# Optimization experiments

Measured on AMD Instinct MI355X. Metric: run time of the kernel, lower is better.

The kernel has to match this reference:

```python
import jax, jax.numpy as jnp
import numpy as np

B, S, D, H = 1, 4096, 1024, 16
HD = D // H  # head_dim = 64


def setup_inputs() -> dict:
    key = jax.random.key(0)
    k1, k2, k3 = jax.random.split(key, 3)
    scale = 0.02
    return {
        "x": jax.random.normal(k1, (B, S, D), dtype=jnp.float32),
        "w_qkv": jax.random.normal(k2, (D, 3 * D), dtype=jnp.float32) * scale,
        "b_qkv": jnp.zeros((3 * D,), dtype=jnp.float32),
        "w_proj": jax.random.normal(k3, (D, D), dtype=jnp.float32) * scale,
        "b_proj": jnp.zeros((D,), dtype=jnp.float32),
    }


def reference(x, w_qkv, b_qkv, w_proj, b_proj):
    b, s, d = x.shape
    qkv = x @ w_qkv + b_qkv                      # [b, s, 3d]
    q, k, v = jnp.split(qkv, 3, axis=-1)
    # [b, h, s, hd]
    q = q.reshape(b, s, H, HD).transpose(0, 2, 1, 3)
    k = k.reshape(b, s, H, HD).transpose(0, 2, 1, 3)
    v = v.reshape(b, s, H, HD).transpose(0, 2, 1, 3)
    score = jnp.einsum("bhqd,bhkd->bhqk", q, k) / jnp.sqrt(jnp.float32(HD))
    causal = jnp.tril(jnp.ones((s, s), dtype=bool))
    score = jnp.where(causal, score, -jnp.inf)
    attn = jax.nn.softmax(score, axis=-1)        # dropout omitted (eval mode, p effectively 0)
    out = jnp.einsum("bhqk,bhkd->bhqd", attn, v)  # [b, h, s, hd]
    out = out.transpose(0, 2, 1, 3).reshape(b, s, d)
    return out @ w_proj + b_proj
```

## Files before the change

kernel.cpp:

```cpp
#include <hip/hip_runtime.h>
#include <hip/hip_bf16.h>
#include <math.h>

typedef __bf16 bf16;
typedef __bf16 bf16x8 __attribute__((ext_vector_type(8)));
typedef __bf16 bf16x4 __attribute__((ext_vector_type(4)));
typedef float f32x4 __attribute__((ext_vector_type(4)));

#define S_ 4096
#define D_ 1024
#define H_ 16
#define HD_ 64
#define N3_ 3072
#define NSPLIT 4

typedef const __attribute__((address_space(1))) void* gas1_t;
typedef __attribute__((address_space(3))) void* las3_t;
static __device__ __forceinline__ void g2l16(const void* g, void* l) {
  __builtin_amdgcn_global_load_lds((gas1_t)g, (las3_t)l, 16, 0, 0);
}

__global__ __launch_bounds__(256) void prep_kernel(const float* __restrict__ x,
                                                   bf16* __restrict__ xb,
                                                   const float* __restrict__ w_qkv,
                                                   bf16* __restrict__ wqkvT,
                                                   const float* __restrict__ w_proj,
                                                   bf16* __restrict__ wprojT) {
  __shared__ float t[32][33];
  const int b = blockIdx.x;
  if (b < 4096) {
    int i = (b * 256 + threadIdx.x) * 4;
    float4 v = *(const float4*)(x + i);
    bf16x4 o;
    o.x = (bf16)v.x; o.y = (bf16)v.y; o.z = (bf16)v.z; o.w = (bf16)v.w;
    *(bf16x4*)(xb + i) = o;
    return;
  }
  const float* in; bf16* outp; int ldin, bx, by;
  if (b < 7168) { int b2 = b - 4096; in = w_qkv;  outp = wqkvT;  ldin = N3_; bx = (b2 % 96) * 32; by = (b2 / 96) * 32; }
  else          { int b3 = b - 7168; in = w_proj; outp = wprojT; ldin = D_;  bx = (b3 % 32) * 32; by = (b3 / 32) * 32; }
  const int tx = threadIdx.x & 31, ty = threadIdx.x >> 5;
#pragma unroll
  for (int i = 0; i < 4; ++i)
    t[ty + i * 8][tx] = in[(size_t)(by + ty + i * 8) * ldin + bx + tx];
  __syncthreads();
#pragma unroll
  for (int i = 0; i < 4; ++i)
    outp[(size_t)(bx + ty + i * 8) * D_ + by + tx] = (bf16)t[tx][ty + i * 8];
}

template <int BN>
__global__ __launch_bounds__(256) void gemm_bt(const bf16* __restrict__ A,
                                               const bf16* __restrict__ Bt,
                                               const float* __restrict__ bias,
                                               bf16* __restrict__ outb,
                                               float* __restrict__ outf,
                                               bf16* __restrict__ vTout,
                                               int M, int N, int K,
                                               int qlim, float qscale) {
  constexpr int NT = BN / 32;
  __shared__ bf16 sA[128 * 32];
  __shared__ bf16 sB[BN * 32];
  const int tid = threadIdx.x;
  const int wave = tid >> 6, lane = tid & 63;
  const int col = lane & 15, quad = lane >> 4;
  const int wm = (wave & 1) * 64, wn = (wave >> 1) * (BN / 2);
  const long bm = (long)blockIdx.x * 128, bn = (long)blockIdx.y * BN;
  const int srow = tid >> 2;
  const int soff = (tid & 3) * 8;

  f32x4 acc[4][NT] = {};

  for (int kb = 0; kb < K; kb += 32) {
    __syncthreads();
    g2l16(A + (bm + srow) * (long)K + kb + soff,      &sA[tid * 8]);
    g2l16(A + (bm + 64 + srow) * (long)K + kb + soff, &sA[2048 + tid * 8]);
#pragma unroll
    for (int i = 0; i < BN / 64; ++i)
      g2l16(Bt + (bn + i * 64 + srow) * (long)K + kb + soff, &sB[i * 2048 + tid * 8]);
    __syncthreads();

    bf16x8 af[4], bfr[NT];
#pragma unroll
    for (int t = 0; t < 4; ++t)
      af[t] = *(const bf16x8*)(&sA[(wm + t * 16 + col) * 32 + quad * 8]);
#pragma unroll
    for (int t = 0; t < NT; ++t)
      bfr[t] = *(const bf16x8*)(&sB[(wn + t * 16 + col) * 32 + quad * 8]);
#pragma unroll
    for (int mt = 0; mt < 4; ++mt)
#pragma unroll
      for (int nt = 0; nt < NT; ++nt)
        acc[mt][nt] = __builtin_amdgcn_mfma_f32_16x16x32_bf16(af[mt], bfr[nt], acc[mt][nt], 0, 0, 0);
  }

#pragma unroll
  for (int mt = 0; mt < 4; ++mt) {
#pragma unroll
    for (int nt = 0; nt < NT; ++nt) {
      long gn = bn + wn + nt * 16 + col;
      float bv = bias ? bias[gn] : 0.f;
      if (vTout && gn >= 2 * D_) {
        bf16x4 vv;
        long gm0 = bm + wm + mt * 16 + quad * 4;
#pragma unroll
        for (int i = 0; i < 4; ++i) vv[i] = (bf16)(acc[mt][nt][i] + bv);
        *(bf16x4*)(&vTout[(gn - 2 * D_) * (long)S_ + gm0]) = vv;
      } else {
        float sc = (gn < qlim) ? qscale : 1.0f;
#pragma unroll
        for (int i = 0; i < 4; ++i) {
          long gm = bm + wm + mt * 16 + quad * 4 + i;
          float v = (acc[mt][nt][i] + bv) * sc;
          if (outf) outf[gm * N + gn] = v;
          else      outb[gm * N + gn] = (bf16)v;
        }
      }
    }
  }
}

__device__ __forceinline__ int swz_g(int row) {
  return (row & 3) | ((((row >> 2) ^ (row >> 3)) & 1) << 2);
}

__global__ __launch_bounds__(256) void attn_kernel(const bf16* __restrict__ qkv,
                                                   const bf16* __restrict__ vT,
                                                   bf16* __restrict__ Opart,
                                                   float* __restrict__ lws) {
  __shared__ bf16 sK[2][64 * 64];
  __shared__ bf16 sV[2][64 * 64];
  const int hh = blockIdx.x;
  const int qb = (int)(gridDim.y - 1 - blockIdx.y);
  const int sp = blockIdx.z;
  const int tid = threadIdx.x;
  const int wave = tid >> 6, lane = tid & 63;
  const int col = lane & 15, quad = lane >> 4;
  const int qbase = qb * 128 + wave * 32;

  const bf16* qp0 = qkv + (size_t)(qbase + col) * N3_ + hh * HD_;
  bf16x8 aq[2][2];
  aq[0][0] = *(const bf16x8*)(qp0 + quad * 8);
  aq[0][1] = *(const bf16x8*)(qp0 + 32 + quad * 8);
  aq[1][0] = *(const bf16x8*)(qp0 + 16 * N3_ + quad * 8);
  aq[1][1] = *(const bf16x8*)(qp0 + 16 * N3_ + 32 + quad * 8);

  bf16x8 ones;
#pragma unroll
  for (int j = 0; j < 8; ++j) ones[j] = (bf16)1.0f;

  f32x4 acc[2][4] = {};
  f32x4 acc_l[2] = {};

  const bf16* kgbase = qkv + D_ + hh * HD_;
  const bf16* vgbase = vT + (size_t)hh * HD_ * S_;
  const int krow = (col >> 2) * 8 + (col & 3);
  const int niter = 2 * (qb + 1);
  const int base = niter >> 2, rem = niter & 3;
  const int it0 = sp * base + (sp < rem ? sp : rem);
  const int len = base + (sp < rem ? 1 : 0);
  const int it1 = it0 + len;

  const int srow = tid >> 2;
  const int sc0 = (tid & 3) * 2;
  const int gs = swz_g(srow);
  const int soff0 = srow * 64 + ((sc0 ^ gs) * 8);
  const int soff1 = srow * 64 + (((sc0 + 1) ^ gs) * 8);

  if (len > 0) {
    {
      const bf16* kg = kgbase + (size_t)(it0 * 64 + srow) * N3_ + sc0 * 8;
      const bf16* vg = vgbase + (size_t)srow * S_ + it0 * 64 + sc0 * 8;
      *(int4*)(&sK[0][soff0]) = *(const int4*)kg;
      *(int4*)(&sK[0][soff1]) = *(const int4*)(kg + 8);
      *(int4*)(&sV[0][soff0]) = *(const int4*)vg;
      *(int4*)(&sV[0][soff1]) = *(const int4*)(vg + 8);
    }
    __syncthreads();

    for (int j = it0; j < it1; ++j) {
      const int kb = j * 64;
      const int cur = (j - it0) & 1;
      const bool more = (j + 1 < it1);
      int4 pk0, pk1, pv0, pv1;
      if (more) {
        const bf16* kg = kgbase + (size_t)(kb + 64 + srow) * N3_ + sc0 * 8;
        const bf16* vg = vgbase + (size_t)srow * S_ + kb + 64 + sc0 * 8;
        pk0 = *(const int4*)kg; pk1 = *(const int4*)(kg + 8);
        pv0 = *(const int4*)vg; pv1 = *(const int4*)(vg + 8);
      }

      if (kb < qbase + 32) {
        const bool act0 = kb < qbase + 16;
        const bf16* kc = &sK[cur][0];
        const bf16* vc = &sV[cur][0];

        f32x4 st[2][4];
#pragma unroll
        for (int t = 0; t < 4; ++t) {
          int row = (t >> 1) * 32 + (t & 1) * 4 + krow;
          int pc = quad ^ swz_g(row);
          bf16x8 bk0 = *(const bf16x8*)(kc + row * 64 + pc * 8);
          bf16x8 bk1 = *(const bf16x8*)(kc + row * 64 + (pc ^ 4) * 8);
          if (act0) {
            f32x4 z = {};
            z = __builtin_amdgcn_mfma_f32_16x16x32_bf16(bk0, aq[0][0], z, 0, 0, 0);
            st[0][t] = __builtin_amdgcn_mfma_f32_16x16x32_bf16(bk1, aq[0][1], z, 0, 0, 0);
          }
          f32x4 z = {};
          z = __builtin_amdgcn_mfma_f32_16x16x32_bf16(bk0, aq[1][0], z, 0, 0, 0);
          st[1][t] = __builtin_amdgcn_mfma_f32_16x16x32_bf16(bk1, aq[1][1], z, 0, 0, 0);
        }

        bf16x8 pfrag[2][2];
#pragma unroll
        for (int s2 = 0; s2 < 2; ++s2) {
          if (s2 == 0 && !act0) continue;
          const int rowbase = qbase + 16 * s2;
          float p[4][4];
          if (kb + 63 <= rowbase) {
#pragma unroll
            for (int t = 0; t < 4; ++t)
#pragma unroll
              for (int r = 0; r < 4; ++r)
                p[t][r] = __builtin_amdgcn_exp2f(st[s2][t][r]);
          } else {
#pragma unroll
            for (int t = 0; t < 4; ++t)
#pragma unroll
              for (int r = 0; r < 4; ++r) {
                int key = kb + (t >> 1) * 32 + quad * 8 + (t & 1) * 4 + r;
                p[t][r] = (key > rowbase + col)
                              ? 0.f
                              : __builtin_amdgcn_exp2f(st[s2][t][r]);
              }
          }
#pragma unroll
          for (int c = 0; c < 2; ++c)
#pragma unroll
            for (int j2 = 0; j2 < 4; ++j2) {
              pfrag[s2][c][j2]     = (bf16)p[2 * c][j2];
              pfrag[s2][c][j2 + 4] = (bf16)p[2 * c + 1][j2];
            }
        }

#pragma unroll
        for (int c = 0; c < 2; ++c) {
#pragma unroll
          for (int n = 0; n < 4; ++n) {
            int row = n * 16 + col;
            int pc = (4 * c + quad) ^ swz_g(row);
            bf16x8 bv = *(const bf16x8*)(vc + row * 64 + pc * 8);
            if (act0)
              acc[0][n] = __builtin_amdgcn_mfma_f32_16x16x32_bf16(pfrag[0][c], bv, acc[0][n], 0, 0, 0);
            acc[1][n] = __builtin_amdgcn_mfma_f32_16x16x32_bf16(pfrag[1][c], bv, acc[1][n], 0, 0, 0);
          }
          if (act0)
            acc_l[0] = __builtin_amdgcn_mfma_f32_16x16x32_bf16(pfrag[0][c], ones, acc_l[0], 0, 0, 0);
          acc_l[1] = __builtin_amdgcn_mfma_f32_16x16x32_bf16(pfrag[1][c], ones, acc_l[1], 0, 0, 0);
        }
      }

      if (more) {
        bf16* kn = &sK[cur ^ 1][0];
        bf16* vn = &sV[cur ^ 1][0];
        *(int4*)(kn + soff0) = pk0;
        *(int4*)(kn + soff1) = pk1;
        *(int4*)(vn + soff0) = pv0;
        *(int4*)(vn + soff1) = pv1;
      }
      __syncthreads();
    }
  }

  bf16* Op = Opart + (size_t)sp * S_ * D_;
#pragma unroll
  for (int s2 = 0; s2 < 2; ++s2) {
    const int rowbase = qbase + 16 * s2;
    if (col == 0) {
#pragma unroll
      for (int r = 0; r < 4; ++r)
        lws[((size_t)sp * H_ + hh) * S_ + rowbase + quad * 4 + r] = acc_l[s2][r];
    }
#pragma unroll
    for (int n = 0; n < 4; ++n)
#pragma unroll
      for (int r = 0; r < 4; ++r)
        Op[(size_t)(rowbase + quad * 4 + r) * D_ + hh * HD_ + n * 16 + col] =
            (bf16)acc[s2][n][r];
  }
}

__global__ __launch_bounds__(256) void attn_combine(const bf16* __restrict__ Opart,
                                                    const float* __restrict__ lws,
                                                    bf16* __restrict__ outb) {
  int e = (blockIdx.x * 256 + threadIdx.x) * 8;
  int s = e >> 10;
  int h = (e & (D_ - 1)) >> 6;
  float l = 0.f;
#pragma unroll
  for (int sp = 0; sp < NSPLIT; ++sp) l += lws[((size_t)sp * H_ + h) * S_ + s];
  float inv = 1.0f / l;
  float o[8] = {};
#pragma unroll
  for (int sp = 0; sp < NSPLIT; ++sp) {
    bf16x8 a = *(const bf16x8*)(Opart + (size_t)sp * S_ * D_ + e);
#pragma unroll
    for (int j = 0; j < 8; ++j) o[j] += (float)a[j];
  }
  bf16x8 r;
#pragma unroll
  for (int j = 0; j < 8; ++j) r[j] = (bf16)(o[j] * inv);
  *(bf16x8*)(outb + e) = r;
}

extern "C" void kernel_launch(void* const* d_in, const int* in_sizes, int n_in,
                              void* d_out, int out_size, void* d_ws, size_t ws_size,
                              hipStream_t stream) {
  const float* x      = (const float*)d_in[0];
  const float* w_qkv  = (const float*)d_in[1];
  const float* b_qkv  = (const float*)d_in[2];
  const float* w_proj = (const float*)d_in[3];
  const float* b_proj = (const float*)d_in[4];
  float* out = (float*)d_out;

  bf16* xb     = (bf16*)d_ws;
  bf16* wqkvT  = xb + (size_t)S_ * D_;
  bf16* wprojT = wqkvT + (size_t)N3_ * D_;
  bf16* qkv    = wprojT + (size_t)D_ * D_;
  bf16* vT     = qkv + (size_t)S_ * N3_;
  bf16* Opart  = vT + (size_t)D_ * S_;
  float* lws   = (float*)(Opart + (size_t)NSPLIT * S_ * D_);
  bf16* attn   = xb;

  const float QSCALE = 0.125f * 1.44269504088896f;

  prep_kernel<<<dim3(8192), 256, 0, stream>>>(x, xb, w_qkv, wqkvT, w_proj, wprojT);
  gemm_bt<128><<<dim3(S_ / 128, N3_ / 128), 256, 0, stream>>>(
      xb, wqkvT, b_qkv, qkv, nullptr, vT, S_, N3_, D_, D_, QSCALE);
  attn_kernel<<<dim3(H_, S_ / 128, NSPLIT), 256, 0, stream>>>(qkv, vT, Opart, lws);
  attn_combine<<<dim3((S_ * D_) / 2048), 256, 0, stream>>>(Opart, lws, attn);
  gemm_bt<64><<<dim3(S_ / 128, D_ / 64), 256, 0, stream>>>(
      attn, wprojT, b_proj, nullptr, out, nullptr, S_, D_, D_, 0, 1.0f);
}
```

Measured before the change: 212.0 us.

## Interleave KV tiles across splits, raise split count to 8, add setprio around MFMA

The attention kernel now splits KV tiles across the split dimension with a stride (round-robin) instead of contiguous chunks. Splits that would get no tiles exit early, and the combine kernel only sums the splits that actually ran. The host picks 8 splits when the workspace is large enough, which gives more blocks for parallelism, but it also means more partial-output traffic in the combine step. s_setprio is raised around the MFMA phases to favour matrix issue over other waves.

```diff
diff --git a/kernel.cpp b/kernel.cpp
--- a/kernel.cpp
+++ b/kernel.cpp
@@ -12,7 +12,6 @@
 #define H_ 16
 #define HD_ 64
 #define N3_ 3072
-#define NSPLIT 4
 
 typedef const __attribute__((address_space(1))) void* gas1_t;
 typedef __attribute__((address_space(3))) void* las3_t;
@@ -133,6 +132,10 @@
   const int hh = blockIdx.x;
   const int qb = (int)(gridDim.y - 1 - blockIdx.y);
   const int sp = blockIdx.z;
+  const int NZ = (int)gridDim.z;
+  const int niter = 2 * (qb + 1);
+  if (sp >= niter) return;
+
   const int tid = threadIdx.x;
   const int wave = tid >> 6, lane = tid & 63;
   const int col = lane & 15, quad = lane >> 4;
@@ -155,11 +158,6 @@
   const bf16* kgbase = qkv + D_ + hh * HD_;
   const bf16* vgbase = vT + (size_t)hh * HD_ * S_;
   const int krow = (col >> 2) * 8 + (col & 3);
-  const int niter = 2 * (qb + 1);
-  const int base = niter >> 2, rem = niter & 3;
-  const int it0 = sp * base + (sp < rem ? sp : rem);
-  const int len = base + (sp < rem ? 1 : 0);
-  const int it1 = it0 + len;
 
   const int srow = tid >> 2;
   const int sc0 = (tid & 3) * 2;
@@ -167,110 +165,112 @@
   const int soff0 = srow * 64 + ((sc0 ^ gs) * 8);
   const int soff1 = srow * 64 + (((sc0 + 1) ^ gs) * 8);
 
-  if (len > 0) {
-    {
-      const bf16* kg = kgbase + (size_t)(it0 * 64 + srow) * N3_ + sc0 * 8;
-      const bf16* vg = vgbase + (size_t)srow * S_ + it0 * 64 + sc0 * 8;
-      *(int4*)(&sK[0][soff0]) = *(const int4*)kg;
-      *(int4*)(&sK[0][soff1]) = *(const int4*)(kg + 8);
-      *(int4*)(&sV[0][soff0]) = *(const int4*)vg;
-      *(int4*)(&sV[0][soff1]) = *(const int4*)(vg + 8);
-    }
-    __syncthreads();
-
-    for (int j = it0; j < it1; ++j) {
-      const int kb = j * 64;
-      const int cur = (j - it0) & 1;
-      const bool more = (j + 1 < it1);
-      int4 pk0, pk1, pv0, pv1;
-      if (more) {
-        const bf16* kg = kgbase + (size_t)(kb + 64 + srow) * N3_ + sc0 * 8;
-        const bf16* vg = vgbase + (size_t)srow * S_ + kb + 64 + sc0 * 8;
-        pk0 = *(const int4*)kg; pk1 = *(const int4*)(kg + 8);
-        pv0 = *(const int4*)vg; pv1 = *(const int4*)(vg + 8);
+  {
+    const bf16* kg = kgbase + (size_t)(sp * 64 + srow) * N3_ + sc0 * 8;
+    const bf16* vg = vgbase + (size_t)srow * S_ + sp * 64 + sc0 * 8;
+    *(int4*)(&sK[0][soff0]) = *(const int4*)kg;
+    *(int4*)(&sK[0][soff1]) = *(const int4*)(kg + 8);
+    *(int4*)(&sV[0][soff0]) = *(const int4*)vg;
+    *(int4*)(&sV[0][soff1]) = *(const int4*)(vg + 8);
+  }
+  __syncthreads();
+
+  int cur = 0;
+  for (int jj = sp; jj < niter; jj += NZ, cur ^= 1) {
+    const int kb = jj * 64;
+    const bool more = (jj + NZ < niter);
+    int4 pk0, pk1, pv0, pv1;
+    if (more) {
+      const bf16* kg = kgbase + (size_t)((jj + NZ) * 64 + srow) * N3_ + sc0 * 8;
+      const bf16* vg = vgbase + (size_t)srow * S_ + (jj + NZ) * 64 + sc0 * 8;
+      pk0 = *(const int4*)kg; pk1 = *(const int4*)(kg + 8);
+      pv0 = *(const int4*)vg; pv1 = *(const int4*)(vg + 8);
+    }
+
+    if (kb < qbase + 32) {
+      const bool act0 = kb < qbase + 16;
+      const bf16* kc = &sK[cur][0];
+      const bf16* vc = &sV[cur][0];
+
+      f32x4 st[2][4];
+      __builtin_amdgcn_s_setprio(1);
+#pragma unroll
+      for (int t = 0; t < 4; ++t) {
+        int row = (t >> 1) * 32 + (t & 1) * 4 + krow;
+        int pc = quad ^ swz_g(row);
+        bf16x8 bk0 = *(const bf16x8*)(kc + row * 64 + pc * 8);
+        bf16x8 bk1 = *(const bf16x8*)(kc + row * 64 + (pc ^ 4) * 8);
+        if (act0) {
+          f32x4 z = {};
+          z = __builtin_amdgcn_mfma_f32_16x16x32_bf16(bk0, aq[0][0], z, 0, 0, 0);
+          st[0][t] = __builtin_amdgcn_mfma_f32_16x16x32_bf16(bk1, aq[0][1], z, 0, 0, 0);
+        }
+        f32x4 z = {};
+        z = __builtin_amdgcn_mfma_f32_16x16x32_bf16(bk0, aq[1][0], z, 0, 0, 0);
+        st[1][t] = __builtin_amdgcn_mfma_f32_16x16x32_bf16(bk1, aq[1][1], z, 0, 0, 0);
       }
-
-      if (kb < qbase + 32) {
-        const bool act0 = kb < qbase + 16;
-        const bf16* kc = &sK[cur][0];
-        const bf16* vc = &sV[cur][0];
-
-        f32x4 st[2][4];
-#pragma unroll
-        for (int t = 0; t < 4; ++t) {
-          int row = (t >> 1) * 32 + (t & 1) * 4 + krow;
-          int pc = quad ^ swz_g(row);
-          bf16x8 bk0 = *(const bf16x8*)(kc + row * 64 + pc * 8);
-          bf16x8 bk1 = *(const bf16x8*)(kc + row * 64 + (pc ^ 4) * 8);
-          if (act0) {
-            f32x4 z = {};
-            z = __builtin_amdgcn_mfma_f32_16x16x32_bf16(bk0, aq[0][0], z, 0, 0, 0);
-            st[0][t] = __builtin_amdgcn_mfma_f32_16x16x32_bf16(bk1, aq[0][1], z, 0, 0, 0);
-          }
-          f32x4 z = {};
-          z = __builtin_amdgcn_mfma_f32_16x16x32_bf16(bk0, aq[1][0], z, 0, 0, 0);
-          st[1][t] = __builtin_amdgcn_mfma_f32_16x16x32_bf16(bk1, aq[1][1], z, 0, 0, 0);
-        }
-
-        bf16x8 pfrag[2][2];
-#pragma unroll
-        for (int s2 = 0; s2 < 2; ++s2) {
-          if (s2 == 0 && !act0) continue;
-          const int rowbase = qbase + 16 * s2;
-          float p[4][4];
-          if (kb + 63 <= rowbase) {
-#pragma unroll
-            for (int t = 0; t < 4; ++t)
-#pragma unroll
-              for (int r = 0; r < 4; ++r)
-                p[t][r] = __builtin_amdgcn_exp2f(st[s2][t][r]);
-          } else {
-#pragma unroll
-            for (int t = 0; t < 4; ++t)
-#pragma unroll
-              for (int r = 0; r < 4; ++r) {
-                int key = kb + (t >> 1) * 32 + quad * 8 + (t & 1) * 4 + r;
-                p[t][r] = (key > rowbase + col)
-                              ? 0.f
-                              : __builtin_amdgcn_exp2f(st[s2][t][r]);
-              }
-          }
-#pragma unroll
-          for (int c = 0; c < 2; ++c)
-#pragma unroll
-            for (int j2 = 0; j2 < 4; ++j2) {
-              pfrag[s2][c][j2]     = (bf16)p[2 * c][j2];
-              pfrag[s2][c][j2 + 4] = (bf16)p[2 * c + 1][j2];
+      __builtin_amdgcn_s_setprio(0);
+
+      bf16x8 pfrag[2][2];
+#pragma unroll
+      for (int s2 = 0; s2 < 2; ++s2) {
+        if (s2 == 0 && !act0) continue;
+        const int rowbase = qbase + 16 * s2;
+        float p[4][4];
+        if (kb + 63 <= rowbase) {
+#pragma unroll
+          for (int t = 0; t < 4; ++t)
+#pragma unroll
+            for (int r = 0; r < 4; ++r)
+              p[t][r] = __builtin_amdgcn_exp2f(st[s2][t][r]);
+        } else {
+#pragma unroll
+          for (int t = 0; t < 4; ++t)
+#pragma unroll
+            for (int r = 0; r < 4; ++r) {
+              int key = kb + (t >> 1) * 32 + quad * 8 + (t & 1) * 4 + r;
+              p[t][r] = (key > rowbase + col)
+                            ? 0.f
+                            : __builtin_amdgcn_exp2f(st[s2][t][r]);
             }
         }
-
-#pragma unroll
-        for (int c = 0; c < 2; ++c) {
-#pragma unroll
-          for (int n = 0; n < 4; ++n) {
-            int row = n * 16 + col;
-            int pc = (4 * c + quad) ^ swz_g(row);
-            bf16x8 bv = *(const bf16x8*)(vc + row * 64 + pc * 8);
-            if (act0)
-              acc[0][n] = __builtin_amdgcn_mfma_f32_16x16x32_bf16(pfrag[0][c], bv, acc[0][n], 0, 0, 0);
-            acc[1][n] = __builtin_amdgcn_mfma_f32_16x16x32_bf16(pfrag[1][c], bv, acc[1][n], 0, 0, 0);
+#pragma unroll
+        for (int c = 0; c < 2; ++c)
+#pragma unroll
+          for (int j2 = 0; j2 < 4; ++j2) {
+            pfrag[s2][c][j2]     = (bf16)p[2 * c][j2];
+            pfrag[s2][c][j2 + 4] = (bf16)p[2 * c + 1][j2];
           }
+      }
+
+      __builtin_amdgcn_s_setprio(1);
+#pragma unroll
+      for (int c = 0; c < 2; ++c) {
+#pragma unroll
+        for (int n = 0; n < 4; ++n) {
+          int row = n * 16 + col;
+          int pc = (4 * c + quad) ^ swz_g(row);
+          bf16x8 bv = *(const bf16x8*)(vc + row * 64 + pc * 8);
           if (act0)
-            acc_l[0] = __builtin_amdgcn_mfma_f32_16x16x32_bf16(pfrag[0][c], ones, acc_l[0], 0, 0, 0);
-          acc_l[1] = __builtin_amdgcn_mfma_f32_16x16x32_bf16(pfrag[1][c], ones, acc_l[1], 0, 0, 0);
+            acc[0][n] = __builtin_amdgcn_mfma_f32_16x16x32_bf16(pfrag[0][c], bv, acc[0][n], 0, 0, 0);
+          acc[1][n] = __builtin_amdgcn_mfma_f32_16x16x32_bf16(pfrag[1][c], bv, acc[1][n], 0, 0, 0);
         }
+        if (act0)
+          acc_l[0] = __builtin_amdgcn_mfma_f32_16x16x32_bf16(pfrag[0][c], ones, acc_l[0], 0, 0, 0);
+        acc_l[1] = __builtin_amdgcn_mfma_f32_16x16x32_bf16(pfrag[1][c], ones, acc_l[1], 0, 0, 0);
       }
-
-      if (more) {
-        bf16* kn = &sK[cur ^ 1][0];
-        bf16* vn = &sV[cur ^ 1][0];
-        *(int4*)(kn + soff0) = pk0;
-        *(int4*)(kn + soff1) = pk1;
-        *(int4*)(vn + soff0) = pv0;
-        *(int4*)(vn + soff1) = pv1;
-      }
-      __syncthreads();
-    }
+      __builtin_amdgcn_s_setprio(0);
+    }
+
+    if (more) {
+      bf16* kn = &sK[cur ^ 1][0];
+      bf16* vn = &sV[cur ^ 1][0];
+      *(int4*)(kn + soff0) = pk0;
+      *(int4*)(kn + soff1) = pk1;
+      *(int4*)(vn + soff0) = pv0;
+      *(int4*)(vn + soff1) = pv1;
+    }
+    __syncthreads();
   }
 
   bf16* Op = Opart + (size_t)sp * S_ * D_;
@@ -293,17 +293,18 @@
 
 __global__ __launch_bounds__(256) void attn_combine(const bf16* __restrict__ Opart,
                                                     const float* __restrict__ lws,
-                                                    bf16* __restrict__ outb) {
+                                                    bf16* __restrict__ outb,
+                                                    int nsplit) {
   int e = (blockIdx.x * 256 + threadIdx.x) * 8;
   int s = e >> 10;
   int h = (e & (D_ - 1)) >> 6;
+  int nit = 2 * ((s >> 7) + 1);
+  int nsp = nsplit < nit ? nsplit : nit;
   float l = 0.f;
-#pragma unroll
-  for (int sp = 0; sp < NSPLIT; ++sp) l += lws[((size_t)sp * H_ + h) * S_ + s];
+  for (int sp = 0; sp < nsp; ++sp) l += lws[((size_t)sp * H_ + h) * S_ + s];
   float inv = 1.0f / l;
   float o[8] = {};
-#pragma unroll
-  for (int sp = 0; sp < NSPLIT; ++sp) {
+  for (int sp = 0; sp < nsp; ++sp) {
     bf16x8 a = *(const bf16x8*)(Opart + (size_t)sp * S_ * D_ + e);
 #pragma unroll
     for (int j = 0; j < 8; ++j) o[j] += (float)a[j];
@@ -324,13 +325,21 @@
   const float* b_proj = (const float*)d_in[4];
   float* out = (float*)d_out;
 
+  const size_t FIXED = (size_t)S_ * D_ * 2
+                     + (size_t)N3_ * D_ * 2
+                     + (size_t)D_ * D_ * 2
+                     + (size_t)S_ * N3_ * 2
+                     + (size_t)D_ * S_ * 2;
+  const size_t PER_SPLIT = (size_t)S_ * D_ * 2 + (size_t)H_ * S_ * 4;
+  const int nsplit = (ws_size >= FIXED + 8 * PER_SPLIT) ? 8 : 4;
+
   bf16* xb     = (bf16*)d_ws;
   bf16* wqkvT  = xb + (size_t)S_ * D_;
   bf16* wprojT = wqkvT + (size_t)N3_ * D_;
   bf16* qkv    = wprojT + (size_t)D_ * D_;
   bf16* vT     = qkv + (size_t)S_ * N3_;
   bf16* Opart  = vT + (size_t)D_ * S_;
-  float* lws   = (float*)(Opart + (size_t)NSPLIT * S_ * D_);
+  float* lws   = (float*)(Opart + (size_t)nsplit * S_ * D_);
   bf16* attn   = xb;
 
   const float QSCALE = 0.125f * 1.44269504088896f;
@@ -338,8 +347,8 @@
   prep_kernel<<<dim3(8192), 256, 0, stream>>>(x, xb, w_qkv, wqkvT, w_proj, wprojT);
   gemm_bt<128><<<dim3(S_ / 128, N3_ / 128), 256, 0, stream>>>(
       xb, wqkvT, b_qkv, qkv, nullptr, vT, S_, N3_, D_, D_, QSCALE);
-  attn_kernel<<<dim3(H_, S_ / 128, NSPLIT), 256, 0, stream>>>(qkv, vT, Opart, lws);
-  attn_combine<<<dim3((S_ * D_) / 2048), 256, 0, stream>>>(Opart, lws, attn);
+  attn_kernel<<<dim3(H_, S_ / 128, nsplit), 256, 0, stream>>>(qkv, vT, Opart, lws);
+  attn_combine<<<dim3((S_ * D_) / 2048), 256, 0, stream>>>(Opart, lws, attn, nsplit);
   gemm_bt<64><<<dim3(S_ / 128, D_ / 64), 256, 0, stream>>>(
       attn, wprojT, b_proj, nullptr, out, nullptr, S_, D_, D_, 0, 1.0f);
 }
```

After: 219.6 us. 1.04x slower.

## Double attention query tile per block and load K/V directly into LDS

Applied to the files above, without the earlier changes.

Each attention block now handles 256 query rows (64 per wave) instead of 128, so every K/V tile staged in shared memory is reused by twice as many queries and the grid shrinks by half. K/V tiles are fetched with direct global-to-LDS loads instead of register staging followed by LDS stores. The KV split becomes an even four-way partition, and wave priority is raised around the MFMA section. In exchange, per-thread accumulator and register use roughly doubles, which risks lower occupancy, and fewer blocks are launched.

```diff
diff --git a/kernel.cpp b/kernel.cpp
--- a/kernel.cpp
+++ b/kernel.cpp
@@ -136,146 +136,131 @@
   const int tid = threadIdx.x;
   const int wave = tid >> 6, lane = tid & 63;
   const int col = lane & 15, quad = lane >> 4;
-  const int qbase = qb * 128 + wave * 32;
+  const int qbase = qb * 256 + wave * 64;
 
   const bf16* qp0 = qkv + (size_t)(qbase + col) * N3_ + hh * HD_;
-  bf16x8 aq[2][2];
-  aq[0][0] = *(const bf16x8*)(qp0 + quad * 8);
-  aq[0][1] = *(const bf16x8*)(qp0 + 32 + quad * 8);
-  aq[1][0] = *(const bf16x8*)(qp0 + 16 * N3_ + quad * 8);
-  aq[1][1] = *(const bf16x8*)(qp0 + 16 * N3_ + 32 + quad * 8);
+  bf16x8 aq[4][2];
+#pragma unroll
+  for (int s2 = 0; s2 < 4; ++s2) {
+    aq[s2][0] = *(const bf16x8*)(qp0 + (size_t)(16 * s2) * N3_ + quad * 8);
+    aq[s2][1] = *(const bf16x8*)(qp0 + (size_t)(16 * s2) * N3_ + 32 + quad * 8);
+  }
 
   bf16x8 ones;
 #pragma unroll
   for (int j = 0; j < 8; ++j) ones[j] = (bf16)1.0f;
 
-  f32x4 acc[2][4] = {};
-  f32x4 acc_l[2] = {};
+  f32x4 acc[4][4] = {};
+  f32x4 acc_l[4] = {};
 
   const bf16* kgbase = qkv + D_ + hh * HD_;
   const bf16* vgbase = vT + (size_t)hh * HD_ * S_;
   const int krow = (col >> 2) * 8 + (col & 3);
-  const int niter = 2 * (qb + 1);
-  const int base = niter >> 2, rem = niter & 3;
-  const int it0 = sp * base + (sp < rem ? sp : rem);
-  const int len = base + (sp < rem ? 1 : 0);
+
+  const int lrow = lane >> 3, lc = lane & 7;
+  const int row0 = wave * 16 + lrow;
+  const int row1 = row0 + 8;
+  const int c0 = lc ^ swz_g(row0);
+  const int c1 = lc ^ swz_g(row1);
+  const int dst0 = wave * 1024 + lane * 8;
+  const int dst1 = dst0 + 512;
+
+  const int niter = 4 * (qb + 1);
+  const int len = niter >> 2;
+  const int it0 = sp * len;
   const int it1 = it0 + len;
 
-  const int srow = tid >> 2;
-  const int sc0 = (tid & 3) * 2;
-  const int gs = swz_g(srow);
-  const int soff0 = srow * 64 + ((sc0 ^ gs) * 8);
-  const int soff1 = srow * 64 + (((sc0 + 1) ^ gs) * 8);
-
-  if (len > 0) {
-    {
-      const bf16* kg = kgbase + (size_t)(it0 * 64 + srow) * N3_ + sc0 * 8;
-      const bf16* vg = vgbase + (size_t)srow * S_ + it0 * 64 + sc0 * 8;
-      *(int4*)(&sK[0][soff0]) = *(const int4*)kg;
-      *(int4*)(&sK[0][soff1]) = *(const int4*)(kg + 8);
-      *(int4*)(&sV[0][soff0]) = *(const int4*)vg;
-      *(int4*)(&sV[0][soff1]) = *(const int4*)(vg + 8);
+  {
+    const int kb2 = it0 * 64;
+    g2l16(kgbase + (size_t)(kb2 + row0) * N3_ + c0 * 8, &sK[0][dst0]);
+    g2l16(kgbase + (size_t)(kb2 + row1) * N3_ + c1 * 8, &sK[0][dst1]);
+    g2l16(vgbase + (size_t)row0 * S_ + kb2 + c0 * 8, &sV[0][dst0]);
+    g2l16(vgbase + (size_t)row1 * S_ + kb2 + c1 * 8, &sV[0][dst1]);
+  }
+  __syncthreads();
+
+  int cur = 0;
+  for (int j = it0; j < it1; ++j, cur ^= 1) {
+    const int kb = j * 64;
+    if (j + 1 < it1) {
+      const int kb2 = kb + 64;
+      const int nb = cur ^ 1;
+      g2l16(kgbase + (size_t)(kb2 + row0) * N3_ + c0 * 8, &sK[nb][dst0]);
+      g2l16(kgbase + (size_t)(kb2 + row1) * N3_ + c1 * 8, &sK[nb][dst1]);
+      g2l16(vgbase + (size_t)row0 * S_ + kb2 + c0 * 8, &sV[nb][dst0]);
+      g2l16(vgbase + (size_t)row1 * S_ + kb2 + c1 * 8, &sV[nb][dst1]);
     }
-    __syncthreads();
-
-    for (int j = it0; j < it1; ++j) {
-      const int kb = j * 64;
-      const int cur = (j - it0) & 1;
-      const bool more = (j + 1 < it1);
-      int4 pk0, pk1, pv0, pv1;
-      if (more) {
-        const bf16* kg = kgbase + (size_t)(kb + 64 + srow) * N3_ + sc0 * 8;
-        const bf16* vg = vgbase + (size_t)srow * S_ + kb + 64 + sc0 * 8;
-        pk0 = *(const int4*)kg; pk1 = *(const int4*)(kg + 8);
-        pv0 = *(const int4*)vg; pv1 = *(const int4*)(vg + 8);
-      }
-
-      if (kb < qbase + 32) {
-        const bool act0 = kb < qbase + 16;
-        const bf16* kc = &sK[cur][0];
-        const bf16* vc = &sV[cur][0];
-
-        f32x4 st[2][4];
-#pragma unroll
-        for (int t = 0; t < 4; ++t) {
-          int row = (t >> 1) * 32 + (t & 1) * 4 + krow;
-          int pc = quad ^ swz_g(row);
-          bf16x8 bk0 = *(const bf16x8*)(kc + row * 64 + pc * 8);
-          bf16x8 bk1 = *(const bf16x8*)(kc + row * 64 + (pc ^ 4) * 8);
-          if (act0) {
+
+    if (kb < qbase + 64) {
+      const bf16* kc = &sK[cur][0];
+      const bf16* vc = &sV[cur][0];
+      bf16x8 pfrag[4][2];
+
+      __builtin_amdgcn_s_setprio(1);
+#pragma unroll
+      for (int t = 0; t < 4; ++t) {
+        const int row = (t >> 1) * 32 + (t & 1) * 4 + krow;
+        const int pc = quad ^ swz_g(row);
+        bf16x8 bk0 = *(const bf16x8*)(kc + row * 64 + pc * 8);
+        bf16x8 bk1 = *(const bf16x8*)(kc + row * 64 + (pc ^ 4) * 8);
+        f32x4 stt[4];
+#pragma unroll
+        for (int s2 = 0; s2 < 4; ++s2) {
+          if (kb < qbase + 16 * s2 + 16) {
             f32x4 z = {};
-            z = __builtin_amdgcn_mfma_f32_16x16x32_bf16(bk0, aq[0][0], z, 0, 0, 0);
-            st[0][t] = __builtin_amdgcn_mfma_f32_16x16x32_bf16(bk1, aq[0][1], z, 0, 0, 0);
+            z = __builtin_amdgcn_mfma_f32_16x16x32_bf16(bk0, aq[s2][0], z, 0, 0, 0);
+            stt[s2] = __builtin_amdgcn_mfma_f32_16x16x32_bf16(bk1, aq[s2][1], z, 0, 0, 0);
           }
-          f32x4 z = {};
-          z = __builtin_amdgcn_mfma_f32_16x16x32_bf16(bk0, aq[1][0], z, 0, 0, 0);
-          st[1][t] = __builtin_amdgcn_mfma_f32_16x16x32_bf16(bk1, aq[1][1], z, 0, 0, 0);
         }
-
-        bf16x8 pfrag[2][2];
-#pragma unroll
-        for (int s2 = 0; s2 < 2; ++s2) {
-          if (s2 == 0 && !act0) continue;
-          const int rowbase = qbase + 16 * s2;
-          float p[4][4];
-          if (kb + 63 <= rowbase) {
-#pragma unroll
-            for (int t = 0; t < 4; ++t)
-#pragma unroll
-              for (int r = 0; r < 4; ++r)
-                p[t][r] = __builtin_amdgcn_exp2f(st[s2][t][r]);
-          } else {
-#pragma unroll
-            for (int t = 0; t < 4; ++t)
+#pragma unroll
+        for (int s2 = 0; s2 < 4; ++s2) {
+          if (kb < qbase + 16 * s2 + 16) {
+            const int rowbase = qbase + 16 * s2;
+            float p[4];
+            if (kb + 63 <= rowbase) {
+#pragma unroll
+              for (int r = 0; r < 4; ++r) p[r] = __builtin_amdgcn_exp2f(stt[s2][r]);
+            } else {
 #pragma unroll
               for (int r = 0; r < 4; ++r) {
                 int key = kb + (t >> 1) * 32 + quad * 8 + (t & 1) * 4 + r;
-                p[t][r] = (key > rowbase + col)
-                              ? 0.f
-                              : __builtin_amdgcn_exp2f(st[s2][t][r]);
+                p[r] = (key > rowbase + col) ? 0.f
+                                             : __builtin_amdgcn_exp2f(stt[s2][r]);
               }
+            }
+#pragma unroll
+            for (int r = 0; r < 4; ++r)
+              pfrag[s2][t >> 1][(t & 1) * 4 + r] = (bf16)p[r];
           }
-#pragma unroll
-          for (int c = 0; c < 2; ++c)
-#pragma unroll
-            for (int j2 = 0; j2 < 4; ++j2) {
-              pfrag[s2][c][j2]     = (bf16)p[2 * c][j2];
-              pfrag[s2][c][j2 + 4] = (bf16)p[2 * c + 1][j2];
-            }
-        }
-
-#pragma unroll
-        for (int c = 0; c < 2; ++c) {
-#pragma unroll
-          for (int n = 0; n < 4; ++n) {
-            int row = n * 16 + col;
-            int pc = (4 * c + quad) ^ swz_g(row);
-            bf16x8 bv = *(const bf16x8*)(vc + row * 64 + pc * 8);
-            if (act0)
-              acc[0][n] = __builtin_amdgcn_mfma_f32_16x16x32_bf16(pfrag[0][c], bv, acc[0][n], 0, 0, 0);
-            acc[1][n] = __builtin_amdgcn_mfma_f32_16x16x32_bf16(pfrag[1][c], bv, acc[1][n], 0, 0, 0);
-          }
-          if (act0)
-            acc_l[0] = __builtin_amdgcn_mfma_f32_16x16x32_bf16(pfrag[0][c], ones, acc_l[0], 0, 0, 0);
-          acc_l[1] = __builtin_amdgcn_mfma_f32_16x16x32_bf16(pfrag[1][c], ones, acc_l[1], 0, 0, 0);
         }
       }
 
-      if (more) {
-        bf16* kn = &sK[cur ^ 1][0];
-        bf16* vn = &sV[cur ^ 1][0];
-        *(int4*)(kn + soff0) = pk0;
-        *(int4*)(kn + soff1) = pk1;
-        *(int4*)(vn + soff0) = pv0;
-        *(int4*)(vn + soff1) = pv1;
+#pragma unroll
+      for (int c = 0; c < 2; ++c) {
+#pragma unroll
+        for (int n = 0; n < 4; ++n) {
+          const int row = n * 16 + col;
+          const int pc = (4 * c + quad) ^ swz_g(row);
+          bf16x8 bv = *(const bf16x8*)(vc + row * 64 + pc * 8);
+#pragma unroll
+          for (int s2 = 0; s2 < 4; ++s2)
+            if (kb < qbase + 16 * s2 + 16)
+              acc[s2][n] = __builtin_amdgcn_mfma_f32_16x16x32_bf16(pfrag[s2][c], bv, acc[s2][n], 0, 0, 0);
+        }
+#pragma unroll
+        for (int s2 = 0; s2 < 4; ++s2)
+          if (kb < qbase + 16 * s2 + 16)
+            acc_l[s2] = __builtin_amdgcn_mfma_f32_16x16x32_bf16(pfrag[s2][c], ones, acc_l[s2], 0, 0, 0);
       }
-      __syncthreads();
+      __builtin_amdgcn_s_setprio(0);
     }
+
+    __syncthreads();
   }
 
   bf16* Op = Opart + (size_t)sp * S_ * D_;
 #pragma unroll
-  for (int s2 = 0; s2 < 2; ++s2) {
+  for (int s2 = 0; s2 < 4; ++s2) {
     const int rowbase = qbase + 16 * s2;
     if (col == 0) {
 #pragma unroll
@@ -338,7 +323,7 @@
   prep_kernel<<<dim3(8192), 256, 0, stream>>>(x, xb, w_qkv, wqkvT, w_proj, wprojT);
   gemm_bt<128><<<dim3(S_ / 128, N3_ / 128), 256, 0, stream>>>(
       xb, wqkvT, b_qkv, qkv, nullptr, vT, S_, N3_, D_, D_, QSCALE);
-  attn_kernel<<<dim3(H_, S_ / 128, NSPLIT), 256, 0, stream>>>(qkv, vT, Opart, lws);
+  attn_kernel<<<dim3(H_, S_ / 256, NSPLIT), 256, 0, stream>>>(qkv, vT, Opart, lws);
   attn_combine<<<dim3((S_ * D_) / 2048), 256, 0, stream>>>(Opart, lws, attn);
   gemm_bt<64><<<dim3(S_ / 128, D_ / 64), 256, 0, stream>>>(
       attn, wprojT, b_proj, nullptr, out, nullptr, S_, D_, D_, 0, 1.0f);
```

New measurement: 239.6 us. 13.0% more time.

## Stream K/V tiles directly to LDS and raise wave priority around MFMA

Applied to the files above, without the earlier changes.

Replaces the register-staged K/V double-buffer prefetch with direct global-to-LDS loads (global_load_lds), remapping the per-lane load layout so the swizzle is applied on the global source side instead of the LDS destination. This removes the VGPRs that held prefetched tiles and the separate LDS store step. The MFMA sections are also bracketed with s_setprio so compute waves get issue priority. A risk is that the final __syncthreads may not wait for the async LDS writes (vmcnt) unless the compiler inserts the wait.

```diff
diff --git a/kernel.cpp b/kernel.cpp
--- a/kernel.cpp
+++ b/kernel.cpp
@@ -161,33 +161,34 @@
   const int len = base + (sp < rem ? 1 : 0);
   const int it1 = it0 + len;
 
-  const int srow = tid >> 2;
-  const int sc0 = (tid & 3) * 2;
-  const int gs = swz_g(srow);
-  const int soff0 = srow * 64 + ((sc0 ^ gs) * 8);
-  const int soff1 = srow * 64 + (((sc0 + 1) ^ gs) * 8);
+  const int lrow = lane >> 3, sl = lane & 7;
+  const int row0 = wave * 8 + lrow;
+  const int row1 = row0 + 32;
+  const int c0 = sl ^ swz_g(row0);
+  const int c1 = sl ^ swz_g(row1);
+  const int dst0 = wave * 512 + lane * 8;
+  const int dst1 = dst0 + 2048;
 
   if (len > 0) {
     {
-      const bf16* kg = kgbase + (size_t)(it0 * 64 + srow) * N3_ + sc0 * 8;
-      const bf16* vg = vgbase + (size_t)srow * S_ + it0 * 64 + sc0 * 8;
-      *(int4*)(&sK[0][soff0]) = *(const int4*)kg;
-      *(int4*)(&sK[0][soff1]) = *(const int4*)(kg + 8);
-      *(int4*)(&sV[0][soff0]) = *(const int4*)vg;
-      *(int4*)(&sV[0][soff1]) = *(const int4*)(vg + 8);
+      const int kb0 = it0 * 64;
+      g2l16(kgbase + (size_t)(kb0 + row0) * N3_ + c0 * 8, &sK[0][dst0]);
+      g2l16(kgbase + (size_t)(kb0 + row1) * N3_ + c1 * 8, &sK[0][dst1]);
+      g2l16(vgbase + (size_t)row0 * S_ + kb0 + c0 * 8, &sV[0][dst0]);
+      g2l16(vgbase + (size_t)row1 * S_ + kb0 + c1 * 8, &sV[0][dst1]);
     }
     __syncthreads();
 
     for (int j = it0; j < it1; ++j) {
       const int kb = j * 64;
       const int cur = (j - it0) & 1;
-      const bool more = (j + 1 < it1);
-      int4 pk0, pk1, pv0, pv1;
-      if (more) {
-        const bf16* kg = kgbase + (size_t)(kb + 64 + srow) * N3_ + sc0 * 8;
-        const bf16* vg = vgbase + (size_t)srow * S_ + kb + 64 + sc0 * 8;
-        pk0 = *(const int4*)kg; pk1 = *(const int4*)(kg + 8);
-        pv0 = *(const int4*)vg; pv1 = *(const int4*)(vg + 8);
+      if (j + 1 < it1) {
+        const int kb2 = kb + 64;
+        const int nb = cur ^ 1;
+        g2l16(kgbase + (size_t)(kb2 + row0) * N3_ + c0 * 8, &sK[nb][dst0]);
+        g2l16(kgbase + (size_t)(kb2 + row1) * N3_ + c1 * 8, &sK[nb][dst1]);
+        g2l16(vgbase + (size_t)row0 * S_ + kb2 + c0 * 8, &sV[nb][dst0]);
+        g2l16(vgbase + (size_t)row1 * S_ + kb2 + c1 * 8, &sV[nb][dst1]);
       }
 
       if (kb < qbase + 32) {
@@ -196,6 +197,7 @@
         const bf16* vc = &sV[cur][0];
 
         f32x4 st[2][4];
+        __builtin_amdgcn_s_setprio(1);
 #pragma unroll
         for (int t = 0; t < 4; ++t) {
           int row = (t >> 1) * 32 + (t & 1) * 4 + krow;
@@ -211,6 +213,7 @@
           z = __builtin_amdgcn_mfma_f32_16x16x32_bf16(bk0, aq[1][0], z, 0, 0, 0);
           st[1][t] = __builtin_amdgcn_mfma_f32_16x16x32_bf16(bk1, aq[1][1], z, 0, 0, 0);
         }
+        __builtin_amdgcn_s_setprio(0);
 
         bf16x8 pfrag[2][2];
 #pragma unroll
@@ -244,6 +247,7 @@
             }
         }
 
+        __builtin_amdgcn_s_setprio(1);
 #pragma unroll
         for (int c = 0; c < 2; ++c) {
 #pragma unroll
@@ -259,16 +263,9 @@
             acc_l[0] = __builtin_amdgcn_mfma_f32_16x16x32_bf16(pfrag[0][c], ones, acc_l[0], 0, 0, 0);
           acc_l[1] = __builtin_amdgcn_mfma_f32_16x16x32_bf16(pfrag[1][c], ones, acc_l[1], 0, 0, 0);
         }
+        __builtin_amdgcn_s_setprio(0);
       }
 
-      if (more) {
-        bf16* kn = &sK[cur ^ 1][0];
-        bf16* vn = &sV[cur ^ 1][0];
-        *(int4*)(kn + soff0) = pk0;
-        *(int4*)(kn + soff1) = pk1;
-        *(int4*)(vn + soff0) = pv0;
-        *(int4*)(vn + soff1) = pv1;
-      }
       __syncthreads();
     }
   }
```

Result: no change. 214.3 us (+1.1%).
